# Performance work log

Hardware: AMD Instinct MI355X
Metric: run time of the kernel (lower is better)

The kernel has to match this reference:

```python
import jax, jax.numpy as jnp
import numpy as np

B, LQ, LK, D = 16, 2048, 2048, 64
EPS = 1e-13
KEEP_PROB = 0.8  # fraction of key positions kept in the mask


def setup_inputs() -> dict:
    key = jax.random.key(0)
    kq, kk, kv, km = jax.random.split(key, 4)
    q = jax.random.normal(kq, (B, LQ, D), dtype=jnp.float32)
    k = jax.random.normal(kk, (B, LK, D), dtype=jnp.float32)
    v = jax.random.normal(kv, (B, LK, D), dtype=jnp.float32)
    # binary 0/1 float mask over key positions (ESIM-style padding mask)
    v_mask = (jax.random.uniform(km, (B, LK)) < KEEP_PROB).astype(jnp.float32)
    return {"q": q, "k": k, "v": v, "v_mask": v_mask}


def masked_softmax(scores, mask):
    # ESIM masked_softmax: softmax(scores * mask) * mask, renormalized.
    m = mask[:, None, :]  # [B, 1, Lk] broadcast over query dim
    p = jax.nn.softmax(scores * m, axis=-1) * m
    return p / (jnp.sum(p, axis=-1, keepdims=True) + EPS)


def reference(q, k, v, v_mask):
    scores = jnp.einsum("bqd,bkd->bqk", q, k)  # [B, Lq, Lk]
    attend = masked_softmax(scores, v_mask)
    return jnp.einsum("bqk,bkd->bqd", attend, v)  # [B, Lq, D]
```

## Files before the change

### kernel.cpp

```cpp
#include <hip/hip_runtime.h>
#include <hip/hip_bf16.h>
#include <stdint.h>

#define NB 16
#define SLQ 2048
#define SLK 2048
#define DD 64
#define BQ 64
#define BK 64
#define NT (SLK / BK)
#define QTILES (SLQ / BQ)
#define LOG2E 1.44269504f

typedef _Float16 f16x8 __attribute__((ext_vector_type(8)));
typedef short s16x8 __attribute__((ext_vector_type(8)));
typedef unsigned short u16x4 __attribute__((ext_vector_type(4)));
typedef float f32x4 __attribute__((ext_vector_type(4)));
typedef float f32x2 __attribute__((ext_vector_type(2)));

typedef __attribute__((address_space(1))) const void gvoid;
typedef __attribute__((address_space(3))) void lvoid;

__device__ __forceinline__ int swzb(int row, int bytecol) {
    return row * 128 + (bytecol ^ ((row & 7) << 4));
}

__device__ __forceinline__ void gload16(const void* g, void* l) {
    __builtin_amdgcn_global_load_lds((gvoid*)g, (lvoid*)l, 16, 0, 0);
}

__device__ __forceinline__ uint16_t f2bf(float f) {
    __bf16 h = (__bf16)f;
    return __builtin_bit_cast(uint16_t, h);
}
__device__ __forceinline__ float bf2f(uint16_t u) {
    uint32_t x = ((uint32_t)u) << 16;
    return __builtin_bit_cast(float, x);
}

__global__ __launch_bounds__(256)
void prep_all(const float* __restrict__ q, const float* __restrict__ k,
              const float* __restrict__ v, const float* __restrict__ vm,
              char* __restrict__ qs, char* __restrict__ ks,
              char* __restrict__ vts, float* __restrict__ bias2) {
    const int bid = blockIdx.x;
    if (bid < 1024) {
        const int tl = bid & 511;
        const bool isq = bid < 512;
        const float sc = isq ? LOG2E : 1.0f;
        const float* src = (isq ? q : k) + (size_t)tl * (BK * DD);
        char* dst = (isq ? qs : ks) + (size_t)tl * (BK * DD * 2);
        #pragma unroll
        for (int it = 0; it < 2; ++it) {
            int c = threadIdx.x + it * 256;
            int row = c >> 3, col8 = c & 7;
            f32x4 a  = *(const f32x4*)(src + row * DD + col8 * 8);
            f32x4 b2 = *(const f32x4*)(src + row * DD + col8 * 8 + 4);
            f16x8 h;
            #pragma unroll
            for (int j = 0; j < 4; ++j) {
                h[j] = (_Float16)(a[j] * sc);
                h[4 + j] = (_Float16)(b2[j] * sc);
            }
            *(f16x8*)(dst + swzb(row, col8 * 16)) = h;
        }
    } else if (bid < 1536) {
        const int tl = bid - 1024;
        const float* src = v + (size_t)tl * (BK * DD);
        char* dst = vts + (size_t)tl * (BK * DD * 2);
        const int d = threadIdx.x & 63;
        #pragma unroll
        for (int it = 0; it < 2; ++it) {
            int key8 = (threadIdx.x >> 6) + it * 4;
            s16x8 h;
            #pragma unroll
            for (int j = 0; j < 8; ++j)
                h[j] = (short)f2bf(src[(key8 * 8 + j) * DD + d]);
            *(s16x8*)(dst + swzb(d, key8 * 16)) = h;
        }
    } else {
        int i = (bid - 1536) * 256 + threadIdx.x;
        bias2[i] = (vm[i] != 0.f) ? 0.f : -2e30f;
    }
}

__global__ __launch_bounds__(256, 4)
void attn_fwd(const char* __restrict__ qs, const char* __restrict__ ks,
              const char* __restrict__ vts, const float* __restrict__ bias2,
              uint16_t* __restrict__ po, float* __restrict__ pl,
              float* __restrict__ out, int nsp)
{
    __shared__ __align__(16) char lp[BQ * DD * 2];
    __shared__ __align__(16) char lk[2][BK * DD * 2];
    __shared__ __align__(16) char lv[2][BK * DD * 2];

    const int tid  = threadIdx.x;
    const int lane = tid & 63;
    const int w    = tid >> 6;
    const int lg   = lane >> 4;
    const int lm   = lane & 15;

    const int G = 512 * nsp;
    int wg = blockIdx.x;
    wg = (wg & 7) * (G >> 3) + (wg >> 3);
    const int qt   = wg & 31;
    const int rest = wg >> 5;
    const int sp   = rest % nsp;
    const int b    = rest / nsp;

    const int qq = NT / nsp, rm = NT % nsp;
    const int t0  = sp * qq + (sp < rm ? sp : rm);
    const int cnt = qq + (sp < rm ? 1 : 0);

    const char* qtile = qs  + (size_t)(b * 32 + qt) * 8192;
    const char* kbase = ks  + (size_t)(b * 32 + t0) * 8192;
    const char* vbase = vts + (size_t)(b * 32 + t0) * 8192;
    const float* mbias = bias2 + (size_t)b * SLK + t0 * BK;

    #pragma unroll
    for (int i = 0; i < 2; ++i) {
        int ch = w * 2 + i;
        gload16(qtile + ch * 1024 + lane * 16, lp + ch * 1024);
    }
    #pragma unroll
    for (int i = 0; i < 2; ++i) {
        int ch = w * 2 + i;
        gload16(kbase + ch * 1024 + lane * 16, lk[0] + ch * 1024);
        gload16(vbase + ch * 1024 + lane * 16, lv[0] + ch * 1024);
    }
    asm volatile("s_waitcnt vmcnt(0)" ::: "memory");
    __syncthreads();

    f16x8 qf[2];
    #pragma unroll
    for (int kc = 0; kc < 2; ++kc)
        qf[kc] = *(const f16x8*)(lp + swzb(w * 16 + lm, kc * 64 + lg * 16));

    s16x8 ones;
    #pragma unroll
    for (int j = 0; j < 8; ++j) ones[j] = (short)0x3F80;

    f32x4 oacc[4], rsacc;
    #pragma unroll
    for (int d = 0; d < 4; ++d) oacc[d] = (f32x4){0.f, 0.f, 0.f, 0.f};
    rsacc = (f32x4){0.f, 0.f, 0.f, 0.f};

    int buf = 0;
    for (int kt = 0; kt < cnt; ++kt) {
        float bv[4];
        #pragma unroll
        for (int f = 0; f < 4; ++f) bv[f] = mbias[kt * BK + f * 16 + lm];

        if (kt + 1 < cnt) {
            const char* kg = kbase + (size_t)(kt + 1) * 8192;
            const char* vg = vbase + (size_t)(kt + 1) * 8192;
            #pragma unroll
            for (int i = 0; i < 2; ++i) {
                int ch = w * 2 + i;
                gload16(kg + ch * 1024 + lane * 16, lk[buf ^ 1] + ch * 1024);
                gload16(vg + ch * 1024 + lane * 16, lv[buf ^ 1] + ch * 1024);
            }
        }

        f32x4 s[4];
        #pragma unroll
        for (int f = 0; f < 4; ++f) s[f] = (f32x4){0.f, 0.f, 0.f, 0.f};
        #pragma unroll
        for (int f = 0; f < 4; ++f) {
            #pragma unroll
            for (int kc = 0; kc < 2; ++kc) {
                f16x8 kf = *(const f16x8*)(lk[buf] + swzb(f * 16 + lm, kc * 64 + lg * 16));
                s[f] = __builtin_amdgcn_mfma_f32_16x16x32_f16(qf[kc], kf, s[f], 0, 0, 0);
            }
        }

        #pragma unroll
        for (int f = 0; f < 4; ++f) {
            #pragma unroll
            for (int i = 0; i < 4; ++i) {
                float p = __builtin_amdgcn_exp2f(s[f][i] + bv[f]);
                *(uint16_t*)(lp + swzb(w * 16 + lg * 4 + i, (f * 16 + lm) * 2)) = f2bf(p);
            }
        }

        #pragma unroll
        for (int kc = 0; kc < 2; ++kc) {
            s16x8 pf = *(const s16x8*)(lp + swzb(w * 16 + lm, kc * 64 + lg * 16));
            rsacc = __builtin_amdgcn_mfma_f32_16x16x32_bf16(pf, ones, rsacc, 0, 0, 0);
            #pragma unroll
            for (int d = 0; d < 4; ++d) {
                s16x8 vf = *(const s16x8*)(lv[buf] + swzb(d * 16 + lm, kc * 64 + lg * 16));
                oacc[d] = __builtin_amdgcn_mfma_f32_16x16x32_bf16(pf, vf, oacc[d], 0, 0, 0);
            }
        }

        asm volatile("s_waitcnt vmcnt(0)" ::: "memory");
        __syncthreads();
        buf ^= 1;
    }

    if (nsp == 1) {
        float* ob = out + ((size_t)b * SLQ + (size_t)qt * BQ) * DD;
        #pragma unroll
        for (int i = 0; i < 4; ++i) {
            float inv = 1.f / (rsacc[i] + 1e-13f);
            int row = w * 16 + lg * 4 + i;
            #pragma unroll
            for (int d = 0; d < 4; ++d)
                ob[row * DD + d * 16 + lm] = oacc[d][i] * inv;
        }
    } else {
        uint16_t* pob = po + (size_t)wg * (BQ * DD);
        #pragma unroll
        for (int i = 0; i < 4; ++i) {
            int row = w * 16 + lg * 4 + i;
            #pragma unroll
            for (int d = 0; d < 4; ++d)
                pob[row * DD + d * 16 + lm] = f2bf(oacc[d][i]);
            if (lm == 0) pl[(size_t)wg * BQ + row] = rsacc[i];
        }
    }
}

__global__ __launch_bounds__(256)
void merge_k(const uint16_t* __restrict__ po, const float* __restrict__ pl,
             float* __restrict__ out, int nsp) {
    const int t  = blockIdx.x;
    const int b  = t >> 5, qt = t & 31;
    const int i0 = (b * nsp) * 32 + qt;
    const int r0 = threadIdx.x >> 4;
    const int c4 = (threadIdx.x & 15) * 4;
    float* ob = out + ((size_t)b * SLQ + (size_t)qt * BQ) * DD;
    #pragma unroll
    for (int rr = 0; rr < BQ; rr += 16) {
        int r = r0 + rr;
        float l = 1e-13f;
        f32x4 acc = (f32x4){0.f, 0.f, 0.f, 0.f};
        for (int s = 0; s < nsp; ++s) {
            int idx = i0 + s * 32;
            l += pl[(size_t)idx * BQ + r];
            u16x4 a = *(const u16x4*)(po + (size_t)idx * (BQ * DD) + r * DD + c4);
            #pragma unroll
            for (int j = 0; j < 4; ++j) acc[j] += bf2f(a[j]);
        }
        float inv = 1.f / l;
        f32x4 o;
        #pragma unroll
        for (int j = 0; j < 4; ++j) o[j] = acc[j] * inv;
        *(f32x4*)(ob + r * DD + c4) = o;
    }
}

__global__ __launch_bounds__(256, 2)
void attn_fallback(const float* __restrict__ q, const float* __restrict__ k,
                   const float* __restrict__ v, const float* __restrict__ vm,
                   float* __restrict__ out)
{
    __shared__ __align__(16) char lqh[64 * DD * 2];
    __shared__ __align__(16) char lql[64 * DD * 2];
    __shared__ __align__(16) char lkh[BK * DD * 2];
    __shared__ __align__(16) char lkl[BK * DD * 2];
    __shared__ __align__(16) char lvt[DD * BK * 2];
    __shared__ __align__(16) char lpp[64 * BK * 2];
    __shared__ float lmask[BK];

    const int tid  = threadIdx.x;
    const int lane = tid & 63;
    const int w    = tid >> 6;
    const int lg   = lane >> 4;
    const int lm   = lane & 15;

    const int b  = blockIdx.y;
    const int qt = blockIdx.x;

    const float* qb = q + ((size_t)b * SLQ + (size_t)qt * 64) * DD;
    const float* kb = k + (size_t)b * SLK * DD;
    const float* vb = v + (size_t)b * SLK * DD;
    const float* mb = vm + (size_t)b * SLK;

    #pragma unroll
    for (int it = 0; it < 2; ++it) {
        int c = tid + it * 256;
        int row = c >> 3, col8 = c & 7;
        f32x4 a  = *(const f32x4*)(qb + row * DD + col8 * 8);
        f32x4 bb = *(const f32x4*)(qb + row * DD + col8 * 8 + 4);
        s16x8 h, l;
        #pragma unroll
        for (int j = 0; j < 4; ++j) {
            uint16_t hh = f2bf(a[j]);
            h[j] = (short)hh; l[j] = (short)f2bf(a[j] - bf2f(hh));
            uint16_t hb = f2bf(bb[j]);
            h[4 + j] = (short)hb; l[4 + j] = (short)f2bf(bb[j] - bf2f(hb));
        }
        *(s16x8*)(lqh + swzb(row, col8 * 16)) = h;
        *(s16x8*)(lql + swzb(row, col8 * 16)) = l;
    }
    __syncthreads();

    s16x8 qfh[2], qfl[2];
    #pragma unroll
    for (int kc = 0; kc < 2; ++kc) {
        qfh[kc] = *(const s16x8*)(lqh + swzb(w * 16 + lm, kc * 64 + lg * 16));
        qfl[kc] = *(const s16x8*)(lql + swzb(w * 16 + lm, kc * 64 + lg * 16));
    }

    float mrow[4], lrow[4];
    f32x4 oacc[4];
    #pragma unroll
    for (int i = 0; i < 4; ++i) { mrow[i] = -1e30f; lrow[i] = 0.f; }
    #pragma unroll
    for (int d = 0; d < 4; ++d) oacc[d] = (f32x4){0.f, 0.f, 0.f, 0.f};

    for (int kt = 0; kt < NT; ++kt) {
        __syncthreads();
        const float* ks2 = kb + (size_t)kt * BK * DD;
        const float* vs = vb + (size_t)kt * BK * DD;

        #pragma unroll
        for (int it = 0; it < 2; ++it) {
            int c = tid + it * 256;
            int row = c >> 3, col8 = c & 7;
            f32x4 a  = *(const f32x4*)(ks2 + row * DD + col8 * 8);
            f32x4 bb = *(const f32x4*)(ks2 + row * DD + col8 * 8 + 4);
            s16x8 h, l;
            #pragma unroll
            for (int j = 0; j < 4; ++j) {
                uint16_t hh = f2bf(a[j]);
                h[j] = (short)hh; l[j] = (short)f2bf(a[j] - bf2f(hh));
                uint16_t hb = f2bf(bb[j]);
                h[4 + j] = (short)hb; l[4 + j] = (short)f2bf(bb[j] - bf2f(hb));
            }
            *(s16x8*)(lkh + swzb(row, col8 * 16)) = h;
            *(s16x8*)(lkl + swzb(row, col8 * 16)) = l;
        }
        #pragma unroll
        for (int it = 0; it < 8; ++it) {
            int c = tid + it * 256;
            int key = c >> 5, dp = (c & 31) * 2;
            f32x2 a = *(const f32x2*)(vs + key * DD + dp);
            *(uint16_t*)(lvt + swzb(dp,     key * 2)) = f2bf(a[0]);
            *(uint16_t*)(lvt + swzb(dp + 1, key * 2)) = f2bf(a[1]);
        }
        if (tid < BK) lmask[tid] = mb[kt * BK + tid];
        __syncthreads();

        f32x4 s[4];
        #pragma unroll
        for (int f = 0; f < 4; ++f) s[f] = (f32x4){0.f, 0.f, 0.f, 0.f};
        #pragma unroll
        for (int f = 0; f < 4; ++f) {
            #pragma unroll
            for (int kc = 0; kc < 2; ++kc) {
                s16x8 kfh = *(const s16x8*)(lkh + swzb(f * 16 + lm, kc * 64 + lg * 16));
                s16x8 kfl = *(const s16x8*)(lkl + swzb(f * 16 + lm, kc * 64 + lg * 16));
                s[f] = __builtin_amdgcn_mfma_f32_16x16x32_bf16(qfh[kc], kfh, s[f], 0, 0, 0);
                s[f] = __builtin_amdgcn_mfma_f32_16x16x32_bf16(qfh[kc], kfl, s[f], 0, 0, 0);
                s[f] = __builtin_amdgcn_mfma_f32_16x16x32_bf16(qfl[kc], kfh, s[f], 0, 0, 0);
            }
        }

        float mv[4];
        #pragma unroll
        for (int f = 0; f < 4; ++f) mv[f] = lmask[f * 16 + lm];

        float pmax[4];
        #pragma unroll
        for (int i = 0; i < 4; ++i) {
            float x = -1e30f;
            #pragma unroll
            for (int f = 0; f < 4; ++f) {
                float sv = (mv[f] != 0.f) ? s[f][i] : -1e30f;
                s[f][i] = sv;
                x = fmaxf(x, sv);
            }
            #pragma unroll
            for (int off = 1; off < 16; off <<= 1)
                x = fmaxf(x, __shfl_xor(x, off, 64));
            pmax[i] = x;
        }

        float scl[4];
        #pragma unroll
        for (int i = 0; i < 4; ++i) {
            float mn = fmaxf(mrow[i], pmax[i]);
            scl[i] = __expf(mrow[i] - mn);
            mrow[i] = mn;
        }
        float rs[4] = {0.f, 0.f, 0.f, 0.f};
        #pragma unroll
        for (int f = 0; f < 4; ++f) {
            #pragma unroll
            for (int i = 0; i < 4; ++i) {
                float p = __expf(s[f][i] - mrow[i]);
                s[f][i] = p;
                rs[i] += p;
            }
        }
        #pragma unroll
        for (int i = 0; i < 4; ++i) {
            #pragma unroll
            for (int off = 1; off < 16; off <<= 1)
                rs[i] += __shfl_xor(rs[i], off, 64);
            lrow[i] = lrow[i] * scl[i] + rs[i];
        }
        #pragma unroll
        for (int d = 0; d < 4; ++d)
            #pragma unroll
            for (int i = 0; i < 4; ++i)
                oacc[d][i] *= scl[i];

        #pragma unroll
        for (int f = 0; f < 4; ++f)
            #pragma unroll
            for (int i = 0; i < 4; ++i)
                *(uint16_t*)(lpp + swzb(w * 16 + lg * 4 + i, (f * 16 + lm) * 2)) = f2bf(s[f][i]);
        __syncthreads();

        #pragma unroll
        for (int kc = 0; kc < 2; ++kc) {
            s16x8 pf = *(const s16x8*)(lpp + swzb(w * 16 + lm, kc * 64 + lg * 16));
            #pragma unroll
            for (int d = 0; d < 4; ++d) {
                s16x8 vf = *(const s16x8*)(lvt + swzb(d * 16 + lm, kc * 64 + lg * 16));
                oacc[d] = __builtin_amdgcn_mfma_f32_16x16x32_bf16(pf, vf, oacc[d], 0, 0, 0);
            }
        }
    }

    float* ob = out + ((size_t)b * SLQ + (size_t)qt * 64) * DD;
    #pragma unroll
    for (int i = 0; i < 4; ++i) {
        float inv = 1.f / (lrow[i] + 1e-13f);
        int row = w * 16 + lg * 4 + i;
        #pragma unroll
        for (int d = 0; d < 4; ++d)
            ob[row * DD + d * 16 + lm] = oacc[d][i] * inv;
    }
}

extern "C" void kernel_launch(void* const* d_in, const int* in_sizes, int n_in,
                              void* d_out, int out_size, void* d_ws, size_t ws_size,
                              hipStream_t stream) {
    const float* q  = (const float*)d_in[0];
    const float* k  = (const float*)d_in[1];
    const float* v  = (const float*)d_in[2];
    const float* vm = (const float*)d_in[3];
    float* out = (float*)d_out;

    const size_t TB     = (size_t)NB * SLK * DD * 2;
    const size_t BIAS   = (size_t)NB * SLK * 4;
    const size_t PL_PER = (size_t)NB * QTILES * BQ * 4;
    const size_t PO_PER = (size_t)NB * QTILES * BQ * DD * 2;
    const size_t base = 3 * TB + BIAS;

    int nsp = 0;
    for (int c = 2; c >= 1; --c) {
        if (ws_size >= base + (size_t)c * (PL_PER + PO_PER)) { nsp = c; break; }
    }
    if (nsp == 0) {
        if (ws_size >= base) nsp = 1;
        else {
            dim3 grid(SLQ / 64, NB);
            attn_fallback<<<grid, dim3(256), 0, stream>>>(q, k, v, vm, out);
            return;
        }
    }

    char*     qs    = (char*)d_ws;
    char*     ks    = qs + TB;
    char*     vts   = ks + TB;
    float*    bias2 = (float*)(vts + TB);
    float*    pl    = (float*)((char*)bias2 + BIAS);
    uint16_t* po    = (uint16_t*)((char*)pl + (size_t)nsp * PL_PER);

    prep_all<<<dim3(1664), dim3(256), 0, stream>>>(q, k, v, vm, qs, ks, vts, bias2);
    attn_fwd<<<dim3(512 * nsp), dim3(256), 0, stream>>>(qs, ks, vts, bias2, po, pl, out, nsp);
    if (nsp > 1)
        merge_k<<<dim3(NB * QTILES), dim3(256), 0, stream>>>(po, pl, out, nsp);
}
```

Baseline: 49.15 us.

## Keep P in registers via transposed QK MFMA and fold mask into V and rowsum

The QK^T MFMA now runs with operands swapped, so each lane's accumulator holds the layout needed for the PV MFMA A-operand. The softmax probabilities are packed into bf16 registers directly, which removes the LDS round-trip for P and the lp buffer. The key mask is no longer an additive bias in the inner loop. Masked keys' V rows are zeroed in prep, and the row sum uses a bf16 0/1 mask vector in place of ones, with key order permuted to match the register layout. This cuts LDS traffic and the bias adds, at the cost of a more intricate key permutation in preprocessing.

```diff
diff --git a/kernel.cpp b/kernel.cpp
--- a/kernel.cpp
+++ b/kernel.cpp
@@ -14,6 +14,7 @@
 
 typedef _Float16 f16x8 __attribute__((ext_vector_type(8)));
 typedef short s16x8 __attribute__((ext_vector_type(8)));
+typedef unsigned int u32x4 __attribute__((ext_vector_type(4)));
 typedef unsigned short u16x4 __attribute__((ext_vector_type(4)));
 typedef float f32x4 __attribute__((ext_vector_type(4)));
 typedef float f32x2 __attribute__((ext_vector_type(2)));
@@ -36,13 +37,17 @@
 __device__ __forceinline__ float bf2f(uint16_t u) {
     uint32_t x = ((uint32_t)u) << 16;
     return __builtin_bit_cast(float, x);
+}
+
+__device__ __forceinline__ int pi64(int x) {
+    return (x & 0x23) | ((x & 4) << 2) | ((x >> 1) & 0x0C);
 }
 
 __global__ __launch_bounds__(256)
 void prep_all(const float* __restrict__ q, const float* __restrict__ k,
               const float* __restrict__ v, const float* __restrict__ vm,
               char* __restrict__ qs, char* __restrict__ ks,
-              char* __restrict__ vts, float* __restrict__ bias2) {
+              char* __restrict__ vts, uint16_t* __restrict__ mb16) {
     const int bid = blockIdx.x;
     if (bid < 1024) {
         const int tl = bid & 511;
@@ -67,6 +72,7 @@
     } else if (bid < 1536) {
         const int tl = bid - 1024;
         const float* src = v + (size_t)tl * (BK * DD);
+        const float* msk = vm + (size_t)tl * BK;
         char* dst = vts + (size_t)tl * (BK * DD * 2);
         const int d = threadIdx.x & 63;
         #pragma unroll
@@ -74,23 +80,31 @@
             int key8 = (threadIdx.x >> 6) + it * 4;
             s16x8 h;
             #pragma unroll
-            for (int j = 0; j < 8; ++j)
-                h[j] = (short)f2bf(src[(key8 * 8 + j) * DD + d]);
+            for (int j = 0; j < 8; ++j) {
+                int kp = key8 * 8 + j;
+                int sk = pi64(kp);
+                float mv = msk[sk];
+                h[j] = (short)f2bf((mv != 0.f) ? src[sk * DD + d] : 0.f);
+            }
             *(s16x8*)(dst + swzb(d, key8 * 16)) = h;
         }
     } else {
-        int i = (bid - 1536) * 256 + threadIdx.x;
-        bias2[i] = (vm[i] != 0.f) ? 0.f : -2e30f;
+        int i = (bid - 1536) * 1024 + threadIdx.x * 4;
+        int srci = (i & ~63) | pi64(i & 63);
+        f32x4 m = *(const f32x4*)(vm + srci);
+        u16x4 o;
+        #pragma unroll
+        for (int j = 0; j < 4; ++j) o[j] = (m[j] != 0.f) ? (uint16_t)0x3F80 : (uint16_t)0;
+        *(u16x4*)(mb16 + i) = o;
     }
 }
 
 __global__ __launch_bounds__(256, 4)
 void attn_fwd(const char* __restrict__ qs, const char* __restrict__ ks,
-              const char* __restrict__ vts, const float* __restrict__ bias2,
+              const char* __restrict__ vts, const uint16_t* __restrict__ mb16,
               uint16_t* __restrict__ po, float* __restrict__ pl,
               float* __restrict__ out, int nsp)
 {
-    __shared__ __align__(16) char lp[BQ * DD * 2];
     __shared__ __align__(16) char lk[2][BK * DD * 2];
     __shared__ __align__(16) char lv[2][BK * DD * 2];
 
@@ -115,12 +129,12 @@
     const char* qtile = qs  + (size_t)(b * 32 + qt) * 8192;
     const char* kbase = ks  + (size_t)(b * 32 + t0) * 8192;
     const char* vbase = vts + (size_t)(b * 32 + t0) * 8192;
-    const float* mbias = bias2 + (size_t)b * SLK + t0 * BK;
+    const uint16_t* mk = mb16 + (size_t)b * SLK + t0 * BK;
 
     #pragma unroll
     for (int i = 0; i < 2; ++i) {
         int ch = w * 2 + i;
-        gload16(qtile + ch * 1024 + lane * 16, lp + ch * 1024);
+        gload16(qtile + ch * 1024 + lane * 16, lk[1] + ch * 1024);
     }
     #pragma unroll
     for (int i = 0; i < 2; ++i) {
@@ -134,11 +148,9 @@
     f16x8 qf[2];
     #pragma unroll
     for (int kc = 0; kc < 2; ++kc)
-        qf[kc] = *(const f16x8*)(lp + swzb(w * 16 + lm, kc * 64 + lg * 16));
-
-    s16x8 ones;
-    #pragma unroll
-    for (int j = 0; j < 8; ++j) ones[j] = (short)0x3F80;
+        qf[kc] = *(const f16x8*)(lk[1] + swzb(w * 16 + lm, kc * 64 + lg * 16));
+    asm volatile("s_waitcnt lgkmcnt(0)" ::: "memory");
+    __syncthreads();
 
     f32x4 oacc[4], rsacc;
     #pragma unroll
@@ -147,9 +159,8 @@
 
     int buf = 0;
     for (int kt = 0; kt < cnt; ++kt) {
-        float bv[4];
-        #pragma unroll
-        for (int f = 0; f < 4; ++f) bv[f] = mbias[kt * BK + f * 16 + lm];
+        s16x8 mf0 = *(const s16x8*)(mk + kt * BK + lg * 8);
+        s16x8 mf1 = *(const s16x8*)(mk + kt * BK + 32 + lg * 8);
 
         if (kt + 1 < cnt) {
             const char* kg = kbase + (size_t)(kt + 1) * 8192;
@@ -170,28 +181,34 @@
             #pragma unroll
             for (int kc = 0; kc < 2; ++kc) {
                 f16x8 kf = *(const f16x8*)(lk[buf] + swzb(f * 16 + lm, kc * 64 + lg * 16));
-                s[f] = __builtin_amdgcn_mfma_f32_16x16x32_f16(qf[kc], kf, s[f], 0, 0, 0);
-            }
-        }
-
+                s[f] = __builtin_amdgcn_mfma_f32_16x16x32_f16(kf, qf[kc], s[f], 0, 0, 0);
+            }
+        }
+
+        uint32_t pw[8];
         #pragma unroll
         for (int f = 0; f < 4; ++f) {
-            #pragma unroll
-            for (int i = 0; i < 4; ++i) {
-                float p = __builtin_amdgcn_exp2f(s[f][i] + bv[f]);
-                *(uint16_t*)(lp + swzb(w * 16 + lg * 4 + i, (f * 16 + lm) * 2)) = f2bf(p);
-            }
-        }
-
-        #pragma unroll
-        for (int kc = 0; kc < 2; ++kc) {
-            s16x8 pf = *(const s16x8*)(lp + swzb(w * 16 + lm, kc * 64 + lg * 16));
-            rsacc = __builtin_amdgcn_mfma_f32_16x16x32_bf16(pf, ones, rsacc, 0, 0, 0);
-            #pragma unroll
-            for (int d = 0; d < 4; ++d) {
-                s16x8 vf = *(const s16x8*)(lv[buf] + swzb(d * 16 + lm, kc * 64 + lg * 16));
-                oacc[d] = __builtin_amdgcn_mfma_f32_16x16x32_bf16(pf, vf, oacc[d], 0, 0, 0);
-            }
+            float p0 = __builtin_amdgcn_exp2f(s[f][0]);
+            float p1 = __builtin_amdgcn_exp2f(s[f][1]);
+            float p2 = __builtin_amdgcn_exp2f(s[f][2]);
+            float p3 = __builtin_amdgcn_exp2f(s[f][3]);
+            pw[f * 2]     = (uint32_t)f2bf(p0) | ((uint32_t)f2bf(p1) << 16);
+            pw[f * 2 + 1] = (uint32_t)f2bf(p2) | ((uint32_t)f2bf(p3) << 16);
+        }
+        u32x4 wa = {pw[0], pw[1], pw[2], pw[3]};
+        u32x4 wb = {pw[4], pw[5], pw[6], pw[7]};
+        s16x8 pa0 = __builtin_bit_cast(s16x8, wa);
+        s16x8 pa1 = __builtin_bit_cast(s16x8, wb);
+
+        rsacc = __builtin_amdgcn_mfma_f32_16x16x32_bf16(pa0, mf0, rsacc, 0, 0, 0);
+        rsacc = __builtin_amdgcn_mfma_f32_16x16x32_bf16(pa1, mf1, rsacc, 0, 0, 0);
+
+        #pragma unroll
+        for (int d = 0; d < 4; ++d) {
+            s16x8 vf0 = *(const s16x8*)(lv[buf] + swzb(d * 16 + lm, lg * 16));
+            s16x8 vf1 = *(const s16x8*)(lv[buf] + swzb(d * 16 + lm, 64 + lg * 16));
+            oacc[d] = __builtin_amdgcn_mfma_f32_16x16x32_bf16(pa0, vf0, oacc[d], 0, 0, 0);
+            oacc[d] = __builtin_amdgcn_mfma_f32_16x16x32_bf16(pa1, vf1, oacc[d], 0, 0, 0);
         }
 
         asm volatile("s_waitcnt vmcnt(0)" ::: "memory");
@@ -448,10 +465,10 @@
     float* out = (float*)d_out;
 
     const size_t TB     = (size_t)NB * SLK * DD * 2;
-    const size_t BIAS   = (size_t)NB * SLK * 4;
+    const size_t MB     = (size_t)NB * SLK * 2;
     const size_t PL_PER = (size_t)NB * QTILES * BQ * 4;
     const size_t PO_PER = (size_t)NB * QTILES * BQ * DD * 2;
-    const size_t base = 3 * TB + BIAS;
+    const size_t base = 3 * TB + MB;
 
     int nsp = 0;
     for (int c = 2; c >= 1; --c) {
@@ -466,15 +483,15 @@
         }
     }
 
-    char*     qs    = (char*)d_ws;
-    char*     ks    = qs + TB;
-    char*     vts   = ks + TB;
-    float*    bias2 = (float*)(vts + TB);
-    float*    pl    = (float*)((char*)bias2 + BIAS);
-    uint16_t* po    = (uint16_t*)((char*)pl + (size_t)nsp * PL_PER);
-
-    prep_all<<<dim3(1664), dim3(256), 0, stream>>>(q, k, v, vm, qs, ks, vts, bias2);
-    attn_fwd<<<dim3(512 * nsp), dim3(256), 0, stream>>>(qs, ks, vts, bias2, po, pl, out, nsp);
+    char*     qs   = (char*)d_ws;
+    char*     ks   = qs + TB;
+    char*     vts  = ks + TB;
+    uint16_t* mb16 = (uint16_t*)(vts + TB);
+    float*    pl   = (float*)((char*)mb16 + MB);
+    uint16_t* po   = (uint16_t*)((char*)pl + (size_t)nsp * PL_PER);
+
+    prep_all<<<dim3(1568), dim3(256), 0, stream>>>(q, k, v, vm, qs, ks, vts, mb16);
+    attn_fwd<<<dim3(512 * nsp), dim3(256), 0, stream>>>(qs, ks, vts, mb16, po, pl, out, nsp);
     if (nsp > 1)
         merge_k<<<dim3(NB * QTILES), dim3(256), 0, stream>>>(po, pl, out, nsp);
 }
```

Result: slower. 50.22 us (+2.2%).
